# Kernel optimization log

Measured on AMD Instinct MI355X. Metric: run time of the kernel, lower is better.

Reference implementation:

```python
import jax, jax.numpy as jnp
import numpy as np

K_CLUSTERS = 512
N_ITERS = 10  # fixed Lloyd iterations (torch_kmeans uses max_iter with tol; fixed count keeps it jit-friendly)


def setup_inputs() -> dict:
    key = jax.random.key(0)
    x = jax.random.normal(key, (4, 8192, 256), dtype=jnp.float32)  # (B, N, D)
    return {"x": x}


def _sq_dists(x, centers):
    # x: (B,N,D), centers: (B,K,D) -> squared Euclidean distances (B,N,K)
    xc = jnp.einsum('bnd,bkd->bnk', x, centers)
    x2 = jnp.sum(x * x, axis=-1, keepdims=True)          # (B,N,1)
    c2 = jnp.sum(centers * centers, axis=-1)[:, None, :]  # (B,1,K)
    return x2 - 2.0 * xc + c2


def _kmeans(x, k=K_CLUSTERS, iters=N_ITERS):
    # deterministic init: first k points of each batch as initial centroids
    centers0 = x[:, :k, :]  # (B,K,D)

    def step(centers, _):
        labels = jnp.argmin(_sq_dists(x, centers), axis=-1)          # (B,N)
        onehot = jax.nn.one_hot(labels, k, dtype=x.dtype)            # (B,N,K)
        sums = jnp.einsum('bnk,bnd->bkd', onehot, x)                 # (B,K,D)
        counts = jnp.sum(onehot, axis=1)                             # (B,K)
        new_centers = jnp.where(
            counts[..., None] > 0,
            sums / jnp.maximum(counts, 1.0)[..., None],
            centers,  # keep empty clusters' previous centroid
        )
        return new_centers, None

    centers, _ = jax.lax.scan(step, centers0, None, length=iters)
    labels = jnp.argmin(_sq_dists(x, centers), axis=-1)
    return labels, centers


def reference(x):
    labels, centers = _kmeans(x)
    return labels, centers
```

## Files before the change

kernel.cpp:

```cpp
#include <hip/hip_runtime.h>
#include <math.h>

#define BB 4
#define NN 8192
#define DD 256
#define KK 512
#define NITERS 10

#define TAU 0.06f
#define NCH 128

typedef _Float16 f16;
typedef f16   f16x8 __attribute__((ext_vector_type(8)));
typedef float f32x4 __attribute__((ext_vector_type(4)));

__global__ __launch_bounds__(256) void init_centers_k(const float* __restrict__ x,
                                                      float* __restrict__ centers,
                                                      f16* __restrict__ chh,
                                                      float* __restrict__ c2) {
    __shared__ float sq[256];
    int bk = blockIdx.x;
    int b  = bk >> 9;
    int k  = bk & 511;
    int t  = threadIdx.x;
    size_t idx = (size_t)bk * DD + t;
    float v = x[((size_t)b * NN + k) * DD + t];
    centers[idx] = v;
    chh[idx] = (f16)v;
    sq[t] = v * v;
    __syncthreads();
    for (int s = 128; s > 0; s >>= 1) {
        if (t < s) sq[t] += sq[t + s];
        __syncthreads();
    }
    if (t == 0) c2[bk] = sq[0];
}

__global__ __launch_bounds__(256) void rowsumsq_k(const float* __restrict__ rows,
                                                  float* __restrict__ out, int nrows) {
    int r = blockIdx.x * 256 + threadIdx.x;
    if (r >= nrows) return;
    const float* p = rows + (size_t)r * DD;
    float total = 0.f;
    #pragma unroll
    for (int h = 0; h < 2; ++h) {
        float a[8];
        #pragma unroll
        for (int j = 0; j < 8; ++j) a[j] = 0.f;
        for (int i = 0; i < 128; i += 8) {
            #pragma unroll
            for (int j = 0; j < 8; ++j) {
                float v  = p[h * 128 + i + j];
                float sq = __fmul_rn(v, v);
                a[j] = __fadd_rn(a[j], sq);
            }
        }
        float s = __fadd_rn(__fadd_rn(__fadd_rn(a[0], a[1]), __fadd_rn(a[2], a[3])),
                            __fadd_rn(__fadd_rn(a[4], a[5]), __fadd_rn(a[6], a[7])));
        total = __fadd_rn(total, s);
    }
    out[r] = total;
}

__global__ __launch_bounds__(256, 2) void assign_k(
    const float* __restrict__ x,
    const f16* __restrict__ chh,
    const float* __restrict__ x2g, const float* __restrict__ c2g,
    int* __restrict__ labels, int* __restrict__ flagslot, int* __restrict__ flaglist)
{
    __shared__ f16 xlh[64 * 256];
    __shared__ f16 xll[64 * 256];
    __shared__ float rv1s[4][64];
    __shared__ float rv2s[4][64];
    __shared__ int   rk1s[4][64];

    const int tid  = threadIdx.x;
    const int wid  = tid >> 6;
    const int lane = tid & 63;
    const int l15  = lane & 15;
    const int lg   = lane >> 4;
    const int b    = blockIdx.x >> 7;
    const int m0   = (blockIdx.x & 127) * 64;

    const float* xb = x + (size_t)(b * NN + m0) * DD;

    #pragma unroll
    for (int i = 0; i < 8; ++i) {
        int lin = tid + i * 256;
        int row = lin >> 5, g = lin & 31;
        const float* p = xb + row * DD + g * 8;
        float4 a  = *(const float4*)p;
        float4 bq = *(const float4*)(p + 4);
        float vf[8] = {a.x, a.y, a.z, a.w, bq.x, bq.y, bq.z, bq.w};
        f16x8 hv, lv;
        #pragma unroll
        for (int j = 0; j < 8; ++j) {
            f16 h = (f16)vf[j];
            hv[j] = h;
            lv[j] = (f16)(vf[j] - (float)h);
        }
        int si = row * 256 + ((g ^ (row & 7)) << 3);
        *(f16x8*)&xlh[si] = hv;
        *(f16x8*)&xll[si] = lv;
    }
    __syncthreads();

    const f16* bhb = chh + ((size_t)b * KK + wid * 128) * DD;

    f32x4 acc[4][8];
    #pragma unroll
    for (int mi = 0; mi < 4; ++mi)
        #pragma unroll
        for (int ki = 0; ki < 8; ++ki)
            acc[mi][ki] = (f32x4){0.f, 0.f, 0.f, 0.f};

    for (int d0 = 0; d0 < DD; d0 += 32) {
        f16x8 ah[4], al[4];
        #pragma unroll
        for (int mi = 0; mi < 4; ++mi) {
            int row = mi * 16 + l15;
            int g   = (d0 >> 3) + lg;
            int si  = row * 256 + ((g ^ (row & 7)) << 3);
            ah[mi] = *(const f16x8*)&xlh[si];
            al[mi] = *(const f16x8*)&xll[si];
        }
        #pragma unroll
        for (int ki = 0; ki < 8; ++ki) {
            size_t off = (size_t)(ki * 16 + l15) * DD + d0 + lg * 8;
            f16x8 bh = *(const f16x8*)(bhb + off);
            #pragma unroll
            for (int mi = 0; mi < 4; ++mi) {
                acc[mi][ki] = __builtin_amdgcn_mfma_f32_16x16x32_f16(ah[mi], bh, acc[mi][ki], 0, 0, 0);
                acc[mi][ki] = __builtin_amdgcn_mfma_f32_16x16x32_f16(al[mi], bh, acc[mi][ki], 0, 0, 0);
            }
        }
    }

    float c2v[8];
    #pragma unroll
    for (int ki = 0; ki < 8; ++ki)
        c2v[ki] = c2g[b * KK + wid * 128 + ki * 16 + l15];

    #pragma unroll
    for (int mi = 0; mi < 4; ++mi) {
        #pragma unroll
        for (int r = 0; r < 4; ++r) {
            int p = mi * 16 + lg * 4 + r;
            float x2p = x2g[b * NN + m0 + p];
            float v1 = __builtin_inff(), v2 = __builtin_inff();
            int   k1 = 0x7fffffff;
            #pragma unroll
            for (int ki = 0; ki < 8; ++ki) {
                float s    = acc[mi][ki][r];
                float cand = __fadd_rn(__fsub_rn(x2p, __fmul_rn(2.0f, s)), c2v[ki]);
                int   kidx = wid * 128 + ki * 16 + l15;
                if (cand < v1 || (cand == v1 && kidx < k1)) { v2 = v1; v1 = cand; k1 = kidx; }
                else if (cand < v2) v2 = cand;
            }
            #pragma unroll
            for (int off = 1; off < 16; off <<= 1) {
                float ov1 = __shfl_xor(v1, off, 64);
                int   ok1 = __shfl_xor(k1, off, 64);
                float ov2 = __shfl_xor(v2, off, 64);
                if (ov1 < v1 || (ov1 == v1 && ok1 < k1)) { v2 = fminf(v1, ov2); v1 = ov1; k1 = ok1; }
                else v2 = fminf(v2, ov1);
            }
            if (l15 == 0) { rv1s[wid][p] = v1; rv2s[wid][p] = v2; rk1s[wid][p] = k1; }
        }
    }
    __syncthreads();
    if (tid < 64) {
        float v1 = rv1s[0][tid], v2 = rv2s[0][tid];
        int   k1 = rk1s[0][tid];
        #pragma unroll
        for (int w = 1; w < 4; ++w) {
            float ov1 = rv1s[w][tid], ov2 = rv2s[w][tid];
            int   ok1 = rk1s[w][tid];
            if (ov1 < v1 || (ov1 == v1 && ok1 < k1)) { v2 = fminf(v1, ov2); v1 = ov1; k1 = ok1; }
            else v2 = fminf(v2, ov1);
        }
        int g = b * NN + m0 + tid;
        labels[g] = k1;
        if (v2 - v1 < TAU) {
            int pos = atomicAdd(flagslot, 1);
            flaglist[pos] = g;
        }
    }
}

__global__ __launch_bounds__(256) void refine_k(const float* __restrict__ x,
                                                const float* __restrict__ centers,
                                                const int* __restrict__ flagslot,
                                                const int* __restrict__ flaglist,
                                                int* __restrict__ labels) {
    __shared__ float  xsr[DD];
    __shared__ double sv[256];
    __shared__ int    si[256];
    const int t = threadIdx.x;
    const int cnt = flagslot[0];
    for (int idx = blockIdx.x; idx < cnt; idx += gridDim.x) {
        const int g = flaglist[idx];
        const int b = g >> 13;
        __syncthreads();
        xsr[t] = x[(size_t)g * DD + t];
        __syncthreads();
        const float* cbase = centers + (size_t)b * KK * DD;
        double bestv = 1e300; int bestk = 0x7fffffff;
        #pragma unroll
        for (int h = 0; h < 2; ++h) {
            int k = t + h * 256;
            const float* cr = cbase + (size_t)k * DD;
            double a0 = 0, a1 = 0, a2 = 0, a3 = 0;
            for (int d = 0; d < DD; d += 4) {
                float4 cv = *(const float4*)(cr + d);
                double f0 = (double)xsr[d + 0] - (double)cv.x;
                double f1 = (double)xsr[d + 1] - (double)cv.y;
                double f2 = (double)xsr[d + 2] - (double)cv.z;
                double f3 = (double)xsr[d + 3] - (double)cv.w;
                a0 += f0 * f0; a1 += f1 * f1; a2 += f2 * f2; a3 += f3 * f3;
            }
            double dist = (a0 + a1) + (a2 + a3);
            if (dist < bestv || (dist == bestv && k < bestk)) { bestv = dist; bestk = k; }
        }
        sv[t] = bestv; si[t] = bestk;
        __syncthreads();
        for (int s = 128; s > 0; s >>= 1) {
            if (t < s) {
                if (sv[t + s] < sv[t] || (sv[t + s] == sv[t] && si[t + s] < si[t])) {
                    sv[t] = sv[t + s]; si[t] = si[t + s];
                }
            }
            __syncthreads();
        }
        if (t == 0) labels[g] = si[0];
    }
}

__global__ __launch_bounds__(64) void chunk_hist_k(const int* __restrict__ labels,
                                                   int* __restrict__ chunkhist) {
    __shared__ int h[KK];
    const int bc = blockIdx.x;
    const int b  = bc >> 7;
    const int c  = bc & (NCH - 1);
    const int t  = threadIdx.x;
    for (int k = t; k < KK; k += 64) h[k] = 0;
    __syncthreads();
    int l = labels[b * NN + c * 64 + t];
    atomicAdd(&h[l], 1);
    __syncthreads();
    int* ch = chunkhist + (size_t)bc * KK;
    for (int k = t; k < KK; k += 64) ch[k] = h[k];
}

__global__ __launch_bounds__(64) void scan_cols_k(int* __restrict__ chunkhist,
                                                  int* __restrict__ counts) {
    const int bq = blockIdx.x;
    const int b  = bq >> 3;
    const int k  = (bq & 7) * 64 + threadIdx.x;
    int* ch = chunkhist + (size_t)b * NCH * KK;
    int run = 0;
    for (int c0 = 0; c0 < NCH; c0 += 16) {
        int v[16];
        #pragma unroll
        for (int j = 0; j < 16; ++j) v[j] = ch[(size_t)(c0 + j) * KK + k];
        #pragma unroll
        for (int j = 0; j < 16; ++j) {
            ch[(size_t)(c0 + j) * KK + k] = run;
            run += v[j];
        }
    }
    counts[b * KK + k] = run;
}

__global__ __launch_bounds__(512) void scan_offsets_k(const int* __restrict__ counts,
                                                      int* __restrict__ offsets) {
    __shared__ int s[KK];
    const int b = blockIdx.x;
    const int k = threadIdx.x;
    int run = counts[b * KK + k];
    s[k] = run;
    __syncthreads();
    for (int off = 1; off < KK; off <<= 1) {
        int v = (k >= off) ? s[k - off] : 0;
        __syncthreads();
        s[k] += v;
        __syncthreads();
    }
    offsets[b * KK + k] = s[k] - run;
}

__global__ __launch_bounds__(64) void scatter_k(const int* __restrict__ labels,
                                                const int* __restrict__ chunkhist,
                                                const int* __restrict__ offsets,
                                                int* __restrict__ idxlist) {
    const int bc = blockIdx.x;
    const int b  = bc >> 7;
    const int c  = bc & (NCH - 1);
    const int t  = threadIdx.x;
    const int n  = c * 64 + t;
    const int l  = labels[b * NN + n];
    int rank = 0;
    for (int j = 0; j < 64; ++j) {
        int lj = __shfl(l, j, 64);
        rank += (lj == l && j < t) ? 1 : 0;
    }
    int base = offsets[b * KK + l] + chunkhist[(size_t)bc * KK + l];
    idxlist[b * NN + base + rank] = n;
}

__global__ __launch_bounds__(1024) void centers_update_k(const float* __restrict__ x,
                                                         float* __restrict__ centers,
                                                         f16* __restrict__ chh,
                                                         float* __restrict__ c2,
                                                         const int* __restrict__ counts,
                                                         const int* __restrict__ offsets,
                                                         const int* __restrict__ idxlist) {
    __shared__ float part[16][DD];
    __shared__ float sq[256];
    const int bk   = blockIdx.x;
    const int b    = bk >> 9;
    const int tid  = threadIdx.x;
    const int w    = tid >> 6;
    const int lane = tid & 63;
    const int cnt = counts[bk];
    if (cnt == 0) return;
    const int* il = idxlist + b * NN + offsets[bk];
    const float* xb = x + (size_t)b * NN * DD;
    float4 acc = {0.f, 0.f, 0.f, 0.f};
    #pragma unroll 4
    for (int j = w; j < cnt; j += 16) {
        int n = il[j];
        float4 v = *(const float4*)(xb + (size_t)n * DD + lane * 4);
        acc.x = __fadd_rn(acc.x, v.x);
        acc.y = __fadd_rn(acc.y, v.y);
        acc.z = __fadd_rn(acc.z, v.z);
        acc.w = __fadd_rn(acc.w, v.w);
    }
    *(float4*)&part[w][lane * 4] = acc;
    __syncthreads();
    float val = 0.f;
    if (tid < DD) {
        float s = 0.f;
        #pragma unroll
        for (int w2 = 0; w2 < 16; ++w2) s = __fadd_rn(s, part[w2][tid]);
        val = s / (float)cnt;
        size_t idx = (size_t)bk * DD + tid;
        centers[idx] = val;
        chh[idx] = (f16)val;
    }
    if (tid < 256) sq[tid] = val * val;
    __syncthreads();
    for (int s = 128; s > 0; s >>= 1) {
        if (tid < s) sq[tid] += sq[tid + s];
        __syncthreads();
    }
    if (tid == 0) c2[bk] = sq[0];
}

__global__ __launch_bounds__(256) void out_k(const int* __restrict__ labels,
                                             const float* __restrict__ centers,
                                             float* __restrict__ out) {
    size_t i = (size_t)blockIdx.x * 256 + threadIdx.x;
    if (i < (size_t)BB * NN) out[i] = (float)labels[i];
    else                     out[i] = centers[i - (size_t)BB * NN];
}

extern "C" void kernel_launch(void* const* d_in, const int* in_sizes, int n_in,
                              void* d_out, int out_size, void* d_ws, size_t ws_size,
                              hipStream_t stream) {
    const float* x = (const float*)d_in[0];
    float* out = (float*)d_out;
    float* ws  = (float*)d_ws;

    float* centers  = ws;
    float* c2       = centers + (size_t)BB * KK * DD;
    float* x2       = c2 + BB * KK;
    int*   labels   = (int*)(x2 + BB * NN);
    int*   flagcnt  = labels + BB * NN;
    int*   flaglist = flagcnt + 64;
    int*   counts   = flaglist + BB * NN;
    int*   offsets  = counts + BB * KK;
    int*   idxlist  = offsets + BB * KK;
    int*   chunkhist= idxlist + BB * NN;
    f16*   chh      = (f16*)(chunkhist + (size_t)BB * NCH * KK);

    hipMemsetAsync(flagcnt, 0, 64 * sizeof(int), stream);

    init_centers_k<<<BB * KK, 256, 0, stream>>>(x, centers, chh, c2);
    rowsumsq_k<<<(BB * NN + 255) / 256, 256, 0, stream>>>(x, x2, BB * NN);

    for (int it = 0; it < NITERS; ++it) {
        assign_k<<<BB * (NN / 64), 256, 0, stream>>>(x, chh, x2, c2,
                                                     labels, flagcnt + it, flaglist);
        refine_k<<<512, 256, 0, stream>>>(x, centers, flagcnt + it, flaglist, labels);
        chunk_hist_k<<<BB * NCH, 64, 0, stream>>>(labels, chunkhist);
        scan_cols_k<<<BB * 8, 64, 0, stream>>>(chunkhist, counts);
        scan_offsets_k<<<BB, 512, 0, stream>>>(counts, offsets);
        scatter_k<<<BB * NCH, 64, 0, stream>>>(labels, chunkhist, offsets, idxlist);
        centers_update_k<<<BB * KK, 1024, 0, stream>>>(x, centers, chh, c2,
                                                       counts, offsets, idxlist);
    }

    assign_k<<<BB * (NN / 64), 256, 0, stream>>>(x, chh, x2, c2,
                                                 labels, flagcnt + NITERS, flaglist);
    refine_k<<<512, 256, 0, stream>>>(x, centers, flagcnt + NITERS, flaglist, labels);

    out_k<<<(int)(((size_t)BB * NN + (size_t)BB * KK * DD + 255) / 256), 256, 0, stream>>>(
        labels, centers, out);
}
```

Before: 956.3 us.

## Enlarge assign tile to 128 points with 8 waves; fuse column and offset scans

The assign kernel now handles 128 points per block using 512 threads (8 waves), with each wave covering 64 centroids rather than 128. Centroid fragments are loaded once per d-step and reused across 8 row tiles, which halves the global centroid reads per point. Shared memory per block doubles to about 128KB, which limits occupancy to one block per CU, and the grid shrinks to 256 blocks. The column scan and offset scan kernels are merged into one launch with 4 blocks, removing a launch but running the column scan with less parallelism.

Measured after the change: 1.003 ms. +4.9%, slower.

```diff
diff --git a/kernel.cpp b/kernel.cpp
--- a/kernel.cpp
+++ b/kernel.cpp
@@ -9,6 +9,7 @@
 
 #define TAU 0.06f
 #define NCH 128
+#define MT 128
 
 typedef _Float16 f16;
 typedef f16   f16x8 __attribute__((ext_vector_type(8)));
@@ -62,31 +63,31 @@
     out[r] = total;
 }
 
-__global__ __launch_bounds__(256, 2) void assign_k(
+__global__ __launch_bounds__(512) void assign_k(
     const float* __restrict__ x,
     const f16* __restrict__ chh,
     const float* __restrict__ x2g, const float* __restrict__ c2g,
     int* __restrict__ labels, int* __restrict__ flagslot, int* __restrict__ flaglist)
 {
-    __shared__ f16 xlh[64 * 256];
-    __shared__ f16 xll[64 * 256];
-    __shared__ float rv1s[4][64];
-    __shared__ float rv2s[4][64];
-    __shared__ int   rk1s[4][64];
+    __shared__ f16 xlh[MT * 256];
+    __shared__ f16 xll[MT * 256];
+    __shared__ float rv1s[8][MT];
+    __shared__ float rv2s[8][MT];
+    __shared__ int   rk1s[8][MT];
 
     const int tid  = threadIdx.x;
     const int wid  = tid >> 6;
     const int lane = tid & 63;
     const int l15  = lane & 15;
     const int lg   = lane >> 4;
-    const int b    = blockIdx.x >> 7;
-    const int m0   = (blockIdx.x & 127) * 64;
+    const int b    = blockIdx.x >> 6;
+    const int m0   = (blockIdx.x & 63) * MT;
 
     const float* xb = x + (size_t)(b * NN + m0) * DD;
 
     #pragma unroll
     for (int i = 0; i < 8; ++i) {
-        int lin = tid + i * 256;
+        int lin = tid + i * 512;
         int row = lin >> 5, g = lin & 31;
         const float* p = xb + row * DD + g * 8;
         float4 a  = *(const float4*)p;
@@ -105,44 +106,44 @@
     }
     __syncthreads();
 
-    const f16* bhb = chh + ((size_t)b * KK + wid * 128) * DD;
-
-    f32x4 acc[4][8];
+    const f16* bhb = chh + ((size_t)b * KK + wid * 64) * DD;
+
+    f32x4 acc[8][4];
     #pragma unroll
-    for (int mi = 0; mi < 4; ++mi)
-        #pragma unroll
-        for (int ki = 0; ki < 8; ++ki)
+    for (int mi = 0; mi < 8; ++mi)
+        #pragma unroll
+        for (int ki = 0; ki < 4; ++ki)
             acc[mi][ki] = (f32x4){0.f, 0.f, 0.f, 0.f};
 
     for (int d0 = 0; d0 < DD; d0 += 32) {
-        f16x8 ah[4], al[4];
-        #pragma unroll
-        for (int mi = 0; mi < 4; ++mi) {
+        f16x8 bh[4];
+        #pragma unroll
+        for (int ki = 0; ki < 4; ++ki) {
+            size_t off = (size_t)(ki * 16 + l15) * DD + d0 + lg * 8;
+            bh[ki] = *(const f16x8*)(bhb + off);
+        }
+        #pragma unroll
+        for (int mi = 0; mi < 8; ++mi) {
             int row = mi * 16 + l15;
             int g   = (d0 >> 3) + lg;
             int si  = row * 256 + ((g ^ (row & 7)) << 3);
-            ah[mi] = *(const f16x8*)&xlh[si];
-            al[mi] = *(const f16x8*)&xll[si];
-        }
-        #pragma unroll
-        for (int ki = 0; ki < 8; ++ki) {
-            size_t off = (size_t)(ki * 16 + l15) * DD + d0 + lg * 8;
-            f16x8 bh = *(const f16x8*)(bhb + off);
+            f16x8 ah = *(const f16x8*)&xlh[si];
+            f16x8 al = *(const f16x8*)&xll[si];
             #pragma unroll
-            for (int mi = 0; mi < 4; ++mi) {
-                acc[mi][ki] = __builtin_amdgcn_mfma_f32_16x16x32_f16(ah[mi], bh, acc[mi][ki], 0, 0, 0);
-                acc[mi][ki] = __builtin_amdgcn_mfma_f32_16x16x32_f16(al[mi], bh, acc[mi][ki], 0, 0, 0);
-            }
-        }
-    }
-
-    float c2v[8];
+            for (int ki = 0; ki < 4; ++ki) {
+                acc[mi][ki] = __builtin_amdgcn_mfma_f32_16x16x32_f16(ah, bh[ki], acc[mi][ki], 0, 0, 0);
+                acc[mi][ki] = __builtin_amdgcn_mfma_f32_16x16x32_f16(al, bh[ki], acc[mi][ki], 0, 0, 0);
+            }
+        }
+    }
+
+    float c2v[4];
     #pragma unroll
-    for (int ki = 0; ki < 8; ++ki)
-        c2v[ki] = c2g[b * KK + wid * 128 + ki * 16 + l15];
+    for (int ki = 0; ki < 4; ++ki)
+        c2v[ki] = c2g[b * KK + wid * 64 + ki * 16 + l15];
 
     #pragma unroll
-    for (int mi = 0; mi < 4; ++mi) {
+    for (int mi = 0; mi < 8; ++mi) {
         #pragma unroll
         for (int r = 0; r < 4; ++r) {
             int p = mi * 16 + lg * 4 + r;
@@ -150,10 +151,10 @@
             float v1 = __builtin_inff(), v2 = __builtin_inff();
             int   k1 = 0x7fffffff;
             #pragma unroll
-            for (int ki = 0; ki < 8; ++ki) {
+            for (int ki = 0; ki < 4; ++ki) {
                 float s    = acc[mi][ki][r];
                 float cand = __fadd_rn(__fsub_rn(x2p, __fmul_rn(2.0f, s)), c2v[ki]);
-                int   kidx = wid * 128 + ki * 16 + l15;
+                int   kidx = wid * 64 + ki * 16 + l15;
                 if (cand < v1 || (cand == v1 && kidx < k1)) { v2 = v1; v1 = cand; k1 = kidx; }
                 else if (cand < v2) v2 = cand;
             }
@@ -169,11 +170,11 @@
         }
     }
     __syncthreads();
-    if (tid < 64) {
+    if (tid < MT) {
         float v1 = rv1s[0][tid], v2 = rv2s[0][tid];
         int   k1 = rk1s[0][tid];
         #pragma unroll
-        for (int w = 1; w < 4; ++w) {
+        for (int w = 1; w < 8; ++w) {
             float ov1 = rv1s[w][tid], ov2 = rv2s[w][tid];
             int   ok1 = rk1s[w][tid];
             if (ov1 < v1 || (ov1 == v1 && ok1 < k1)) { v2 = fminf(v1, ov2); v1 = ov1; k1 = ok1; }
@@ -252,11 +253,12 @@
     for (int k = t; k < KK; k += 64) ch[k] = h[k];
 }
 
-__global__ __launch_bounds__(64) void scan_cols_k(int* __restrict__ chunkhist,
-                                                  int* __restrict__ counts) {
-    const int bq = blockIdx.x;
-    const int b  = bq >> 3;
-    const int k  = (bq & 7) * 64 + threadIdx.x;
+__global__ __launch_bounds__(512) void scan_k(int* __restrict__ chunkhist,
+                                              int* __restrict__ counts,
+                                              int* __restrict__ offsets) {
+    __shared__ int s[KK];
+    const int b = blockIdx.x;
+    const int k = threadIdx.x;
     int* ch = chunkhist + (size_t)b * NCH * KK;
     int run = 0;
     for (int c0 = 0; c0 < NCH; c0 += 16) {
@@ -270,14 +272,6 @@
         }
     }
     counts[b * KK + k] = run;
-}
-
-__global__ __launch_bounds__(512) void scan_offsets_k(const int* __restrict__ counts,
-                                                      int* __restrict__ offsets) {
-    __shared__ int s[KK];
-    const int b = blockIdx.x;
-    const int k = threadIdx.x;
-    int run = counts[b * KK + k];
     s[k] = run;
     __syncthreads();
     for (int off = 1; off < KK; off <<= 1) {
@@ -390,18 +384,17 @@
     rowsumsq_k<<<(BB * NN + 255) / 256, 256, 0, stream>>>(x, x2, BB * NN);
 
     for (int it = 0; it < NITERS; ++it) {
-        assign_k<<<BB * (NN / 64), 256, 0, stream>>>(x, chh, x2, c2,
+        assign_k<<<BB * (NN / MT), 512, 0, stream>>>(x, chh, x2, c2,
                                                      labels, flagcnt + it, flaglist);
         refine_k<<<512, 256, 0, stream>>>(x, centers, flagcnt + it, flaglist, labels);
         chunk_hist_k<<<BB * NCH, 64, 0, stream>>>(labels, chunkhist);
-        scan_cols_k<<<BB * 8, 64, 0, stream>>>(chunkhist, counts);
-        scan_offsets_k<<<BB, 512, 0, stream>>>(counts, offsets);
+        scan_k<<<BB, 512, 0, stream>>>(chunkhist, counts, offsets);
         scatter_k<<<BB * NCH, 64, 0, stream>>>(labels, chunkhist, offsets, idxlist);
         centers_update_k<<<BB * KK, 1024, 0, stream>>>(x, centers, chh, c2,
                                                        counts, offsets, idxlist);
     }
 
-    assign_k<<<BB * (NN / 64), 256, 0, stream>>>(x, chh, x2, c2,
+    assign_k<<<BB * (NN / MT), 512, 0, stream>>>(x, chh, x2, c2,
                                                  labels, flagcnt + NITERS, flaglist);
     refine_k<<<512, 256, 0, stream>>>(x, centers, flagcnt + NITERS, flaglist, labels);
 
```
